# Kernel optimization log

Measured on AMD Instinct MI355X. Metric: run time of the kernel, lower is better.

Reference implementation:

```python
import jax, jax.numpy as jnp
import numpy as np


def _cos_map(N):
    # DCT-II basis: weight[n, x] = cos(n*(x+0.5)/N*pi)*sqrt(2/N), row 0 scaled by 1/sqrt(2)
    pos = (jnp.arange(N, dtype=jnp.float32) + 0.5) / N
    n = jnp.arange(N, dtype=jnp.float32)[:, None]
    w = jnp.cos(n * pos[None, :] * jnp.pi) * np.sqrt(2.0 / N)
    return w.at[0].multiply(1.0 / np.sqrt(2.0))


def _dct3(x, cT, cH, cW):
    # x: [B,C,T,H,W]; matmul(x, cos.T) along each axis
    x = jnp.einsum('bcthw,Ww->bcthW', x, cW)
    x = jnp.einsum('bcthw,Hh->bctHw', x, cH)
    x = jnp.einsum('bcthw,Tt->bcThw', x, cT)
    return x


def _idct3(x, cT, cH, cW):
    # matmul(x, cos) along each axis
    x = jnp.einsum('bcthw,wW->bcthW', x, cW)
    x = jnp.einsum('bcthw,hH->bctHw', x, cH)
    x = jnp.einsum('bcthw,tT->bcThw', x, cT)
    return x


def setup_inputs() -> dict:
    key = jax.random.key(0)
    ks = jax.random.split(key, 12)
    B, C, T, H, W = 2, 96, 16, 64, 64
    hd = 96
    s = 0.02
    return {
        'x': jax.random.normal(ks[0], (B, C, T, H, W), jnp.float32),
        'freq_embed': jax.random.normal(ks[1], (T, H, W, hd), jnp.float32),
        'dwconv_w': jax.random.normal(ks[2], (hd, 1, 3, 3, 3), jnp.float32) * s,
        'dwconv_b': jnp.zeros((hd,), jnp.float32),
        'linear_w': jax.random.normal(ks[3], (2 * hd, hd), jnp.float32) * s,
        'linear_b': jnp.zeros((2 * hd,), jnp.float32),
        'v0_w': jax.random.normal(ks[4], (hd, hd), jnp.float32) * s,
        'v0_b': jnp.zeros((hd,), jnp.float32),
        'tok_w': jax.random.normal(ks[5], (hd, hd), jnp.float32) * s,
        'tok_b': jnp.zeros((hd,), jnp.float32),
        'c': jnp.ones((1,), jnp.float32),
        'alpha': jnp.full((1,), 0.1, jnp.float32),
        'ln_g': jnp.ones((hd,), jnp.float32),
        'ln_b': jnp.zeros((hd,), jnp.float32),
        'out_w': jax.random.normal(ks[6], (hd, hd), jnp.float32) * s,
        'out_b': jnp.zeros((hd,), jnp.float32),
    }


def reference(x, freq_embed, dwconv_w, dwconv_b, linear_w, linear_b, v0_w, v0_b,
              tok_w, tok_b, c, alpha, ln_g, ln_b, out_w, out_b):
    B, C, T, H, W = x.shape
    hd = C
    # depthwise 3x3x3 conv
    y = jax.lax.conv_general_dilated(
        x, dwconv_w, (1, 1, 1), [(1, 1)] * 3,
        dimension_numbers=('NCDHW', 'OIDHW', 'NCDHW'), feature_group_count=hd)
    y = y + dwconv_b[None, :, None, None, None]
    yl = jnp.moveaxis(y, 1, -1)                     # [B,T,H,W,C]
    lin = yl @ linear_w.T + linear_b                # [B,T,H,W,2C]
    xg, z = jnp.split(lin, 2, axis=-1)
    v0 = xg @ v0_w.T + v0_b
    xc = jnp.moveaxis(xg, -1, 1)                    # [B,C,T,H,W]
    v0c = jnp.moveaxis(v0, -1, 1)
    cT, cH, cW = _cos_map(T), _cos_map(H), _cos_map(W)
    x_u0 = _dct3(xc, cT, cH, cW)
    x_v0 = _dct3(v0c, cT, cH, cW)
    # tau from freq_embed (exact GELU, as torch default)
    tau = jax.nn.gelu(freq_embed @ tok_w.T + tok_b, approximate=False)  # [T,H,W,C]
    tau = jnp.moveaxis(tau, -1, 0)[None]            # [1,C,T,H,W] broadcasts over B
    c_tau = c[0] * tau
    damping = jnp.exp(-alpha[0] / 2 * tau)
    spec = damping * (jnp.cos(c_tau) * x_u0 +
                      jnp.sin(c_tau) / (c[0] + 1e-8) * (x_v0 + alpha[0] / 2 * x_u0))
    xf = _idct3(spec, cT, cH, cW)
    xf = jnp.moveaxis(xf, 1, -1)                    # [B,T,H,W,C]
    mu = xf.mean(-1, keepdims=True)
    var = ((xf - mu) ** 2).mean(-1, keepdims=True)
    xf = (xf - mu) / jnp.sqrt(var + 1e-5) * ln_g + ln_b
    xf = xf * jax.nn.silu(z)                        # elementwise gate
    out = xf @ out_w.T + out_b
    return jnp.moveaxis(out, -1, 1)                 # [B,C,T,H,W]
```

## Files before the change

### kernel.cpp

```cpp
#include <hip/hip_runtime.h>
#include <math.h>

#define THW 65536
#define HW  4096
#define C96 96
#ifndef M_PI
#define M_PI 3.14159265358979323846
#endif

__global__ __launch_bounds__(256) void init_basis_k(float* __restrict__ b64,
                                                    float* __restrict__ b64T,
                                                    float* __restrict__ b16) {
  int tid = threadIdx.x;
  for (int i = tid; i < 4096; i += 256) {
    int n = i >> 6, x = i & 63;
    double s = sqrt(2.0 / 64.0) * (n == 0 ? sqrt(0.5) : 1.0);
    float v = (float)(cos((double)n * ((double)x + 0.5) * M_PI / 64.0) * s);
    b64[i] = v;
    b64T[x * 64 + n] = v;
  }
  {
    int n = tid >> 4, x = tid & 15;
    double s = sqrt(2.0 / 16.0) * (n == 0 ? sqrt(0.5) : 1.0);
    b16[tid & 255] = (float)(cos((double)n * ((double)x + 0.5) * M_PI / 16.0) * s);
  }
}

__global__ __launch_bounds__(256) void dwconv_k(const float* __restrict__ x,
    const float* __restrict__ wv, const float* __restrict__ bias,
    float* __restrict__ y) {
  __shared__ float lds[4 * 66 * 72];
  int tid = threadIdx.x;
  int t0 = blockIdx.x * 2;
  int bc = blockIdx.y;
  int c  = bc % C96;
  const float* xp = x + (size_t)bc * THW;

  float4 z4 = make_float4(0.f, 0.f, 0.f, 0.f);
  for (int i = tid; i < 4752; i += 256) ((float4*)lds)[i] = z4;
  __syncthreads();
  for (int p = 0; p < 4; ++p) {
    int tt = t0 - 1 + p;
    if (tt < 0 || tt > 15) continue;
    const float* pp = xp + tt * HW;
    for (int i = tid; i < 1024; i += 256) {
      int row = i >> 4, c4 = i & 15;
      float4 v = *(const float4*)(pp + row * 64 + c4 * 4);
      *(float4*)&lds[(p * 66 + row + 1) * 72 + 4 + c4 * 4] = v;
    }
  }
  float w27[27];
#pragma unroll
  for (int i = 0; i < 27; ++i) w27[i] = wv[c * 27 + i];
  float bv = bias[c];
  __syncthreads();

  int s   = tid & 7;
  int tc  = (tid >> 3) & 1;
  int seg = tid >> 4;
  int h0 = seg * 4;
  int cb = 3 + 8 * s;

  float win[3][3][10];
#define LOADROW(q, slot, ldsrow) { \
    const float* rp = &lds[(((tc) + (q)) * 66 + (ldsrow)) * 72 + cb]; \
    _Pragma("unroll") for (int j = 0; j < 10; ++j) win[q][slot][j] = rp[j]; }

#pragma unroll
  for (int q = 0; q < 3; ++q) { LOADROW(q, 0, h0); LOADROW(q, 1, h0 + 1); }

  float* yp = y + (size_t)bc * THW + (t0 + tc) * HW + s * 8;
#pragma unroll
  for (int st = 0; st < 4; ++st) {
    int h = h0 + st;
#pragma unroll
    for (int q = 0; q < 3; ++q) { LOADROW(q, (st + 2) % 3, h + 2); }
    float acc[8];
#pragma unroll
    for (int w = 0; w < 8; ++w) acc[w] = bv;
#pragma unroll
    for (int q = 0; q < 3; ++q)
#pragma unroll
      for (int rr = 0; rr < 3; ++rr) {
        const float* row = win[q][(st + rr) % 3];
#pragma unroll
        for (int dw = 0; dw < 3; ++dw) {
          float coef = w27[q * 9 + rr * 3 + dw];
#pragma unroll
          for (int w = 0; w < 8; ++w) acc[w] = fmaf(row[w + dw], coef, acc[w]);
        }
      }
    *(float4*)&yp[h * 64]     = make_float4(acc[0], acc[1], acc[2], acc[3]);
    *(float4*)&yp[h * 64 + 4] = make_float4(acc[4], acc[5], acc[6], acc[7]);
  }
#undef LOADROW
}

__global__ __launch_bounds__(256) void feT_k(const float* __restrict__ fe,
                                             float* __restrict__ feT) {
  __shared__ float t[96 * 65];
  int tid = threadIdx.x;
  int tok0 = blockIdx.x * 64;
  const float* p = fe + (size_t)tok0 * 96;
  for (int i = tid; i < 6144; i += 256) {
    int tok = i / 96;
    int ch = i - tok * 96;
    t[ch * 65 + tok] = p[i];
  }
  __syncthreads();
  for (int i = tid; i < 6144; i += 256) {
    int ch = i >> 6, tok = i & 63;
    feT[(size_t)ch * THW + tok0 + tok] = t[ch * 65 + tok];
  }
}

#define FMA4(A, WV) \
  A.x = fmaf(WV, v.x, A.x); A.y = fmaf(WV, v.y, A.y); \
  A.z = fmaf(WV, v.z, A.z); A.w = fmaf(WV, v.w, A.w);

#define WPAD 104
#define BK32 32

template <int EPI>
__global__ __launch_bounds__(512) void gemm96_k(
    const float* __restrict__ In, const float* __restrict__ W,
    const float* __restrict__ bias, float* __restrict__ Out,
    float* __restrict__ Out2, const float* __restrict__ zg,
    const float* __restrict__ lnG, const float* __restrict__ lnB,
    const float* __restrict__ scal_c, const float* __restrict__ scal_a,
    int N, size_t inStride, size_t outStride) {
  __shared__ float Wt[96 * WPAD];
  __shared__ float buf[BK32 * 256];
  int tid = threadIdx.x;
  int wvi = tid >> 6, ln = tid & 63;
  for (int i = tid; i < 2304; i += 512) {
    int k4 = i / 96, co = i - k4 * 96;
    float4 w4 = *(const float4*)(W + co * 96 + k4 * 4);
    int k = k4 * 4;
    Wt[(k + 0) * WPAD + co] = w4.x;
    Wt[(k + 1) * WPAD + co] = w4.y;
    Wt[(k + 2) * WPAD + co] = w4.z;
    Wt[(k + 3) * WPAD + co] = w4.w;
  }
  int n0 = blockIdx.x * 256 + ln * 4;
  int co0 = wvi * 12;
  const float* ipb = In + blockIdx.y * inStride + blockIdx.x * 256 + ln * 4;
  const float* zpb = (EPI == 2) ? (zg + blockIdx.y * inStride + blockIdx.x * 256 + ln * 4)
                                : nullptr;

  float4 mu4, rs4;
  if (EPI == 2) {
    float4 sum = make_float4(0.f, 0.f, 0.f, 0.f);
    float4 sq  = make_float4(0.f, 0.f, 0.f, 0.f);
#pragma unroll 8
    for (int ci = 0; ci < 96; ++ci) {
      float4 t = *(const float4*)(ipb + (size_t)ci * N);
      sum.x += t.x; sum.y += t.y; sum.z += t.z; sum.w += t.w;
      sq.x = fmaf(t.x, t.x, sq.x); sq.y = fmaf(t.y, t.y, sq.y);
      sq.z = fmaf(t.z, t.z, sq.z); sq.w = fmaf(t.w, t.w, sq.w);
    }
    const float r96 = 1.0f / 96.0f;
    mu4.x = sum.x * r96; mu4.y = sum.y * r96; mu4.z = sum.z * r96; mu4.w = sum.w * r96;
    rs4.x = rsqrtf(fmaxf(sq.x * r96 - mu4.x * mu4.x, 0.f) + 1e-5f);
    rs4.y = rsqrtf(fmaxf(sq.y * r96 - mu4.y * mu4.y, 0.f) + 1e-5f);
    rs4.z = rsqrtf(fmaxf(sq.z * r96 - mu4.z * mu4.z, 0.f) + 1e-5f);
    rs4.w = rsqrtf(fmaxf(sq.w * r96 - mu4.w * mu4.w, 0.f) + 1e-5f);
  }

  float4 acc[12];
#pragma unroll
  for (int j = 0; j < 12; ++j) {
    float bj = bias[co0 + j];
    acc[j] = make_float4(bj, bj, bj, bj);
  }

#pragma unroll 1
  for (int kb = 0; kb < 3; ++kb) {
#pragma unroll
    for (int i = 0; i < 4; ++i) {
      int r = i * 8 + wvi;
      int k = kb * BK32 + r;
      float4 v4 = *(const float4*)(ipb + (size_t)k * N);
      if (EPI == 2) {
        float4 zz = *(const float4*)(zpb + (size_t)k * N);
        float lgk = lnG[k], lbk = lnB[k];
        float gx = zz.x * __builtin_amdgcn_rcpf(1.0f + __expf(-zz.x));
        float gy = zz.y * __builtin_amdgcn_rcpf(1.0f + __expf(-zz.y));
        float gz = zz.z * __builtin_amdgcn_rcpf(1.0f + __expf(-zz.z));
        float gw = zz.w * __builtin_amdgcn_rcpf(1.0f + __expf(-zz.w));
        v4.x = fmaf((v4.x - mu4.x) * rs4.x, lgk, lbk) * gx;
        v4.y = fmaf((v4.y - mu4.y) * rs4.y, lgk, lbk) * gy;
        v4.z = fmaf((v4.z - mu4.z) * rs4.z, lgk, lbk) * gz;
        v4.w = fmaf((v4.w - mu4.w) * rs4.w, lgk, lbk) * gw;
      }
      *(float4*)&buf[r * 256 + ln * 4] = v4;
    }
    __syncthreads();
#pragma unroll 8
    for (int kk = 0; kk < BK32; ++kk) {
      int k = kb * BK32 + kk;
      float4 v = *(const float4*)&buf[kk * 256 + ln * 4];
      const float4* wr = (const float4*)&Wt[k * WPAD + co0];
#pragma unroll
      for (int j = 0; j < 3; ++j) {
        float4 wvv = wr[j];
        FMA4(acc[4 * j + 0], wvv.x);
        FMA4(acc[4 * j + 1], wvv.y);
        FMA4(acc[4 * j + 2], wvv.z);
        FMA4(acc[4 * j + 3], wvv.w);
      }
    }
    __syncthreads();
  }

  if (EPI == 1) {
    float cv = scal_c[0], al = scal_a[0];
    float rc = 1.0f / (cv + 1e-8f);
#define TAUMAP(T, AA, BB) { \
    float tau = 0.5f * (T) * (1.0f + erff((T) * 0.70710678118654752f)); \
    float ct = cv * tau; \
    float damp = __expf(-0.5f * al * tau); \
    float sc = __sinf(ct), cc = __cosf(ct); \
    AA = damp * (cc + sc * al * 0.5f * rc); BB = damp * sc * rc; }
#pragma unroll 2
    for (int j = 0; j < 12; ++j) {
      float4 a4, b4;
      TAUMAP(acc[j].x, a4.x, b4.x);
      TAUMAP(acc[j].y, a4.y, b4.y);
      TAUMAP(acc[j].z, a4.z, b4.z);
      TAUMAP(acc[j].w, a4.w, b4.w);
      *(float4*)(Out  + (size_t)(co0 + j) * N + n0) = a4;
      *(float4*)(Out2 + (size_t)(co0 + j) * N + n0) = b4;
    }
#undef TAUMAP
  } else {
    float* op = Out + blockIdx.y * outStride + n0;
#pragma unroll
    for (int j = 0; j < 12; ++j)
      *(float4*)(op + (size_t)(co0 + j) * N) = acc[j];
  }
}

__global__ __launch_bounds__(256) void wh_k(const float* __restrict__ in,
    float* __restrict__ out, const float* __restrict__ basis) {
  __shared__ float XT[64 * 68];
  __shared__ float Yb[64 * 68];
  __shared__ float Bs[64 * 68];
  int tid = threadIdx.x;
  const float* ip = in + (size_t)blockIdx.x * HW;
  float* op = out + (size_t)blockIdx.x * HW;
  for (int i = tid; i < 1024; i += 256) {
    int r = i >> 4, c4 = i & 15;
    float4 v = *(const float4*)(basis + r * 64 + c4 * 4);
    *(float4*)&Bs[r * 68 + c4 * 4] = v;
  }
  for (int i = tid; i < 1024; i += 256) {
    int h = i >> 4, w4 = i & 15;
    float4 v = *(const float4*)(ip + h * 64 + w4 * 4);
    int w = w4 * 4;
    XT[(w + 0) * 68 + h] = v.x;
    XT[(w + 1) * 68 + h] = v.y;
    XT[(w + 2) * 68 + h] = v.z;
    XT[(w + 3) * 68 + h] = v.w;
  }
  __syncthreads();
  int nb = tid & 15, rb = tid >> 4;
  int n0 = nb * 4, r0 = rb * 4;
  {
    float4 a0 = make_float4(0.f, 0.f, 0.f, 0.f), a1 = a0, a2 = a0, a3 = a0;
#pragma unroll 8
    for (int w = 0; w < 64; ++w) {
      float4 xv = *(const float4*)&XT[w * 68 + r0];
      float4 bv = *(const float4*)&Bs[w * 68 + n0];
      a0.x = fmaf(xv.x, bv.x, a0.x); a0.y = fmaf(xv.x, bv.y, a0.y);
      a0.z = fmaf(xv.x, bv.z, a0.z); a0.w = fmaf(xv.x, bv.w, a0.w);
      a1.x = fmaf(xv.y, bv.x, a1.x); a1.y = fmaf(xv.y, bv.y, a1.y);
      a1.z = fmaf(xv.y, bv.z, a1.z); a1.w = fmaf(xv.y, bv.w, a1.w);
      a2.x = fmaf(xv.z, bv.x, a2.x); a2.y = fmaf(xv.z, bv.y, a2.y);
      a2.z = fmaf(xv.z, bv.z, a2.z); a2.w = fmaf(xv.z, bv.w, a2.w);
      a3.x = fmaf(xv.w, bv.x, a3.x); a3.y = fmaf(xv.w, bv.y, a3.y);
      a3.z = fmaf(xv.w, bv.z, a3.z); a3.w = fmaf(xv.w, bv.w, a3.w);
    }
    *(float4*)&Yb[(r0 + 0) * 68 + n0] = a0;
    *(float4*)&Yb[(r0 + 1) * 68 + n0] = a1;
    *(float4*)&Yb[(r0 + 2) * 68 + n0] = a2;
    *(float4*)&Yb[(r0 + 3) * 68 + n0] = a3;
  }
  __syncthreads();
  {
    float4 a0 = make_float4(0.f, 0.f, 0.f, 0.f), a1 = a0, a2 = a0, a3 = a0;
#pragma unroll 8
    for (int h = 0; h < 64; ++h) {
      float4 bv = *(const float4*)&Bs[h * 68 + r0];
      float4 yv = *(const float4*)&Yb[h * 68 + n0];
      a0.x = fmaf(bv.x, yv.x, a0.x); a0.y = fmaf(bv.x, yv.y, a0.y);
      a0.z = fmaf(bv.x, yv.z, a0.z); a0.w = fmaf(bv.x, yv.w, a0.w);
      a1.x = fmaf(bv.y, yv.x, a1.x); a1.y = fmaf(bv.y, yv.y, a1.y);
      a1.z = fmaf(bv.y, yv.z, a1.z); a1.w = fmaf(bv.y, yv.w, a1.w);
      a2.x = fmaf(bv.z, yv.x, a2.x); a2.y = fmaf(bv.z, yv.y, a2.y);
      a2.z = fmaf(bv.z, yv.z, a2.z); a2.w = fmaf(bv.z, yv.w, a2.w);
      a3.x = fmaf(bv.w, yv.x, a3.x); a3.y = fmaf(bv.w, yv.y, a3.y);
      a3.z = fmaf(bv.w, yv.z, a3.z); a3.w = fmaf(bv.w, yv.w, a3.w);
    }
    *(float4*)&op[(r0 + 0) * 64 + n0] = a0;
    *(float4*)&op[(r0 + 1) * 64 + n0] = a1;
    *(float4*)&op[(r0 + 2) * 64 + n0] = a2;
    *(float4*)&op[(r0 + 3) * 64 + n0] = a3;
  }
}

__global__ __launch_bounds__(256) void tspec_k(const float* __restrict__ U0,
    const float* __restrict__ V0, const float* __restrict__ A,
    const float* __restrict__ Bc, const float* __restrict__ b16,
    float* __restrict__ out) {
  __shared__ float bs[256];
  int tid = threadIdx.x;
  bs[tid] = b16[tid];
  __syncthreads();
  int hw = blockIdx.x * 256 + tid;
  int c = blockIdx.y, b = blockIdx.z;
  size_t base = ((size_t)(b * C96 + c) * 16) * HW + hw;
  int cbase = c * THW + hw;
  float ua[16], va[16];
  {
    float u[16];
#pragma unroll
    for (int t = 0; t < 16; ++t) u[t] = U0[base + t * HW];
#pragma unroll
    for (int n = 0; n < 16; ++n) {
      float s = 0.0f;
#pragma unroll
      for (int t = 0; t < 16; ++t) s = fmaf(bs[n * 16 + t], u[t], s);
      ua[n] = s;
    }
  }
  {
    float v[16];
#pragma unroll
    for (int t = 0; t < 16; ++t) v[t] = V0[base + t * HW];
#pragma unroll
    for (int n = 0; n < 16; ++n) {
      float s = 0.0f;
#pragma unroll
      for (int t = 0; t < 16; ++t) s = fmaf(bs[n * 16 + t], v[t], s);
      va[n] = s;
    }
  }
  float so[16];
#pragma unroll 4
  for (int n = 0; n < 16; ++n)
    so[n] = A[cbase + n * HW] * ua[n] + Bc[cbase + n * HW] * va[n];
#pragma unroll
  for (int t = 0; t < 16; ++t) {
    float s = 0.0f;
#pragma unroll
    for (int n = 0; n < 16; ++n) s = fmaf(so[n], bs[n * 16 + t], s);
    out[base + t * HW] = s;
  }
}

extern "C" void kernel_launch(void* const* d_in, const int* in_sizes, int n_in,
                              void* d_out, int out_size, void* d_ws, size_t ws_size,
                              hipStream_t stream) {
  const float* x    = (const float*)d_in[0];
  const float* fe   = (const float*)d_in[1];
  const float* dww  = (const float*)d_in[2];
  const float* dwb  = (const float*)d_in[3];
  const float* linW = (const float*)d_in[4];
  const float* linB = (const float*)d_in[5];
  const float* v0W  = (const float*)d_in[6];
  const float* v0B  = (const float*)d_in[7];
  const float* tokW = (const float*)d_in[8];
  const float* tokB = (const float*)d_in[9];
  const float* cS   = (const float*)d_in[10];
  const float* aS   = (const float*)d_in[11];
  const float* lnG  = (const float*)d_in[12];
  const float* lnBp = (const float*)d_in[13];
  const float* outW = (const float*)d_in[14];
  const float* outB = (const float*)d_in[15];
  float* out = (float*)d_out;

  float* w = (float*)d_ws;
  const size_t TEN = (size_t)2 * C96 * THW;
  const size_t BST = (size_t)C96 * THW;
  float* b64    = w;
  float* b64T   = w + 4096;
  float* b16    = w + 8192;
  float* buf_y  = w + 16384;
  float* buf_xg = buf_y + TEN;
  float* buf_z  = buf_xg + TEN;
  float* buf_v0 = buf_z + TEN;
  float* bufA   = buf_v0 + TEN;
  float* bufB   = bufA + BST;
  size_t need = (size_t)(16384 + 4 * TEN + 2 * BST) * sizeof(float);
  if (ws_size < need) return;

  hipLaunchKernelGGL(init_basis_k, dim3(1), dim3(256), 0, stream, b64, b64T, b16);
  hipLaunchKernelGGL(dwconv_k, dim3(8, 192), dim3(256), 0, stream, x, dww, dwb, buf_y);
  hipLaunchKernelGGL((gemm96_k<0>), dim3(256, 2), dim3(512), 0, stream,
                     buf_y, linW, linB, buf_xg, (float*)nullptr, (const float*)nullptr,
                     (const float*)nullptr, (const float*)nullptr,
                     (const float*)nullptr, (const float*)nullptr, THW, BST, BST);
  hipLaunchKernelGGL((gemm96_k<0>), dim3(256, 2), dim3(512), 0, stream,
                     buf_y, linW + 9216, linB + 96, buf_z, (float*)nullptr, (const float*)nullptr,
                     (const float*)nullptr, (const float*)nullptr,
                     (const float*)nullptr, (const float*)nullptr, THW, BST, BST);
  hipLaunchKernelGGL(feT_k, dim3(1024), dim3(256), 0, stream, fe, buf_v0);
  hipLaunchKernelGGL((gemm96_k<1>), dim3(256, 1), dim3(512), 0, stream,
                     buf_v0, tokW, tokB, bufA, bufB, (const float*)nullptr,
                     (const float*)nullptr, (const float*)nullptr,
                     cS, aS, THW, (size_t)0, (size_t)0);
  hipLaunchKernelGGL((gemm96_k<0>), dim3(256, 2), dim3(512), 0, stream,
                     buf_xg, v0W, v0B, buf_v0, (float*)nullptr, (const float*)nullptr,
                     (const float*)nullptr, (const float*)nullptr,
                     (const float*)nullptr, (const float*)nullptr, THW, BST, BST);
  hipLaunchKernelGGL(wh_k, dim3(3072), dim3(256), 0, stream, buf_xg, buf_y, b64T);
  hipLaunchKernelGGL(wh_k, dim3(3072), dim3(256), 0, stream, buf_v0, buf_xg, b64T);
  hipLaunchKernelGGL(tspec_k, dim3(16, 96, 2), dim3(256), 0, stream, buf_y, buf_xg, bufA, bufB, b16, buf_v0);
  hipLaunchKernelGGL(wh_k, dim3(3072), dim3(256), 0, stream, buf_v0, buf_y, b64);
  hipLaunchKernelGGL((gemm96_k<2>), dim3(256, 2), dim3(512), 0, stream,
                     buf_y, outW, outB, out, (float*)nullptr, buf_z,
                     lnG, lnBp, (const float*)nullptr, (const float*)nullptr, THW, BST, BST);
}
```

Baseline: 617.3 us.

## Rewrite depthwise conv as LDS-free register-streaming kernel with wave shuffles

The depthwise 3x3x3 conv kernel no longer stages a zero-padded tile in shared memory. Each wave now owns one time slice and a 32-row stripe. Each lane holds one column and streams rows from the three neighbouring time planes directly from global memory. Horizontal neighbours are exchanged with wave shuffles, and the time boundary is handled by zeroing weights. The goal is to remove the LDS fill, the barriers and the LDS read traffic, at the cost of scalar (non-vector) global loads and stores and repeated global reads of halo planes.

```diff
diff --git a/kernel.cpp b/kernel.cpp
--- a/kernel.cpp
+++ b/kernel.cpp
@@ -26,75 +26,85 @@
   }
 }
 
+struct R3 { float a, b, c; };
+
+#define LOADR(dst, row) { int rr_ = (row); int o_ = rr_ * 64 + lane; \
+    dst.a = pmv[o_]; dst.b = pcv[o_]; dst.c = ppv[o_]; }
+
+#define OUTROW(A, B, Cc, row) { \
+    float P0, P1, P2; \
+    P0 = w27[0]  * A.a;          P1 = w27[1]  * A.a;          P2 = w27[2]  * A.a; \
+    P0 = fmaf(w27[3],  B.a, P0); P1 = fmaf(w27[4],  B.a, P1); P2 = fmaf(w27[5],  B.a, P2); \
+    P0 = fmaf(w27[6],  Cc.a, P0); P1 = fmaf(w27[7],  Cc.a, P1); P2 = fmaf(w27[8],  Cc.a, P2); \
+    P0 = fmaf(w27[9],  A.b, P0); P1 = fmaf(w27[10], A.b, P1); P2 = fmaf(w27[11], A.b, P2); \
+    P0 = fmaf(w27[12], B.b, P0); P1 = fmaf(w27[13], B.b, P1); P2 = fmaf(w27[14], B.b, P2); \
+    P0 = fmaf(w27[15], Cc.b, P0); P1 = fmaf(w27[16], Cc.b, P1); P2 = fmaf(w27[17], Cc.b, P2); \
+    P0 = fmaf(w27[18], A.c, P0); P1 = fmaf(w27[19], A.c, P1); P2 = fmaf(w27[20], A.c, P2); \
+    P0 = fmaf(w27[21], B.c, P0); P1 = fmaf(w27[22], B.c, P1); P2 = fmaf(w27[23], B.c, P2); \
+    P0 = fmaf(w27[24], Cc.c, P0); P1 = fmaf(w27[25], Cc.c, P1); P2 = fmaf(w27[26], Cc.c, P2); \
+    float lft = __shfl_up(P0, 1);  if (lane == 0)  lft = 0.f; \
+    float rgt = __shfl_down(P2, 1); if (lane == 63) rgt = 0.f; \
+    yp[(row) * 64] = bv + lft + P1 + rgt; }
+
 __global__ __launch_bounds__(256) void dwconv_k(const float* __restrict__ x,
     const float* __restrict__ wv, const float* __restrict__ bias,
     float* __restrict__ y) {
-  __shared__ float lds[4 * 66 * 72];
-  int tid = threadIdx.x;
-  int t0 = blockIdx.x * 2;
-  int bc = blockIdx.y;
-  int c  = bc % C96;
-  const float* xp = x + (size_t)bc * THW;
-
-  float4 z4 = make_float4(0.f, 0.f, 0.f, 0.f);
-  for (int i = tid; i < 4752; i += 256) ((float4*)lds)[i] = z4;
-  __syncthreads();
-  for (int p = 0; p < 4; ++p) {
-    int tt = t0 - 1 + p;
-    if (tt < 0 || tt > 15) continue;
-    const float* pp = xp + tt * HW;
-    for (int i = tid; i < 1024; i += 256) {
-      int row = i >> 4, c4 = i & 15;
-      float4 v = *(const float4*)(pp + row * 64 + c4 * 4);
-      *(float4*)&lds[(p * 66 + row + 1) * 72 + 4 + c4 * 4] = v;
-    }
-  }
+  int lane = threadIdx.x & 63;
+  int wvi  = threadIdx.x >> 6;
+  int bc   = blockIdx.x;
+  int t    = blockIdx.y * 4 + wvi;
+  int h0   = blockIdx.z * 32;
+  int c    = bc % C96;
+
+  const float* pcv = x + (size_t)bc * THW + (size_t)t * HW;
+  const float* pmv = (t > 0)  ? pcv - HW : pcv;
+  const float* ppv = (t < 15) ? pcv + HW : pcv;
+
   float w27[27];
 #pragma unroll
   for (int i = 0; i < 27; ++i) w27[i] = wv[c * 27 + i];
+  if (t == 0) {
+#pragma unroll
+    for (int i = 0; i < 9; ++i) w27[i] = 0.f;
+  }
+  if (t == 15) {
+#pragma unroll
+    for (int i = 0; i < 9; ++i) w27[18 + i] = 0.f;
+  }
   float bv = bias[c];
-  __syncthreads();
-
-  int s   = tid & 7;
-  int tc  = (tid >> 3) & 1;
-  int seg = tid >> 4;
-  int h0 = seg * 4;
-  int cb = 3 + 8 * s;
-
-  float win[3][3][10];
-#define LOADROW(q, slot, ldsrow) { \
-    const float* rp = &lds[(((tc) + (q)) * 66 + (ldsrow)) * 72 + cb]; \
-    _Pragma("unroll") for (int j = 0; j < 10; ++j) win[q][slot][j] = rp[j]; }
-
-#pragma unroll
-  for (int q = 0; q < 3; ++q) { LOADROW(q, 0, h0); LOADROW(q, 1, h0 + 1); }
-
-  float* yp = y + (size_t)bc * THW + (t0 + tc) * HW + s * 8;
-#pragma unroll
-  for (int st = 0; st < 4; ++st) {
-    int h = h0 + st;
-#pragma unroll
-    for (int q = 0; q < 3; ++q) { LOADROW(q, (st + 2) % 3, h + 2); }
-    float acc[8];
-#pragma unroll
-    for (int w = 0; w < 8; ++w) acc[w] = bv;
-#pragma unroll
-    for (int q = 0; q < 3; ++q)
-#pragma unroll
-      for (int rr = 0; rr < 3; ++rr) {
-        const float* row = win[q][(st + rr) % 3];
-#pragma unroll
-        for (int dw = 0; dw < 3; ++dw) {
-          float coef = w27[q * 9 + rr * 3 + dw];
-#pragma unroll
-          for (int w = 0; w < 8; ++w) acc[w] = fmaf(row[w + dw], coef, acc[w]);
-        }
-      }
-    *(float4*)&yp[h * 64]     = make_float4(acc[0], acc[1], acc[2], acc[3]);
-    *(float4*)&yp[h * 64 + 4] = make_float4(acc[4], acc[5], acc[6], acc[7]);
-  }
-#undef LOADROW
-}
+  float* yp = y + (size_t)bc * THW + (size_t)t * HW + lane;
+
+  R3 s0, s1, s2, s3, n0, n1;
+  if (h0 > 0) { LOADR(s0, h0 - 1) } else { s0.a = s0.b = s0.c = 0.f; }
+  LOADR(s1, h0)
+  LOADR(s2, h0 + 1)
+  LOADR(s3, h0 + 2)
+#pragma unroll
+  for (int p = 0; p < 14; ++p) {
+    int h = h0 + 2 * p;
+    LOADR(n0, h + 3)
+    LOADR(n1, h + 4)
+    OUTROW(s0, s1, s2, h)
+    OUTROW(s1, s2, s3, h + 1)
+    s0 = s2; s1 = s3; s2 = n0; s3 = n1;
+  }
+  {
+    int h = h0 + 28;
+    LOADR(n0, h + 3)
+    if (h0 == 0) { LOADR(n1, h + 4) }
+    else { n1.a = n1.b = n1.c = 0.f; }
+    OUTROW(s0, s1, s2, h)
+    OUTROW(s1, s2, s3, h + 1)
+    s0 = s2; s1 = s3; s2 = n0; s3 = n1;
+  }
+  {
+    int h = h0 + 30;
+    OUTROW(s0, s1, s2, h)
+    OUTROW(s1, s2, s3, h + 1)
+  }
+}
+#undef LOADR
+#undef OUTROW
 
 __global__ __launch_bounds__(256) void feT_k(const float* __restrict__ fe,
                                              float* __restrict__ feT) {
@@ -396,7 +406,7 @@
   if (ws_size < need) return;
 
   hipLaunchKernelGGL(init_basis_k, dim3(1), dim3(256), 0, stream, b64, b64T, b16);
-  hipLaunchKernelGGL(dwconv_k, dim3(8, 192), dim3(256), 0, stream, x, dww, dwb, buf_y);
+  hipLaunchKernelGGL(dwconv_k, dim3(192, 4, 2), dim3(256), 0, stream, x, dww, dwb, buf_y);
   hipLaunchKernelGGL((gemm96_k<0>), dim3(256, 2), dim3(512), 0, stream,
                      buf_y, linW, linB, buf_xg, (float*)nullptr, (const float*)nullptr,
                      (const float*)nullptr, (const float*)nullptr,
```

Measured after the change: 570.6 us. -7.6%, faster.
